# Performance work log

Hardware: AMD Instinct MI355X
Metric: run time of the kernel (lower is better)

## Reference

```python
import jax, jax.numpy as jnp
import numpy as np

# Architecture constants (from RUMamba.__init__ hard-coded Mamba2 config)
D_MODEL = 512
D_STATE = 128
D_CONV = 4
EXPAND = 4
HEADDIM = 32
D_INNER = EXPAND * D_MODEL            # 2048
NHEADS = D_INNER // HEADDIM           # 64
CONV_DIM = D_INNER + 2 * D_STATE      # 2304 (ngroups=1)
D_IN_PROJ = 2 * D_INNER + 2 * D_STATE + NHEADS  # 4416
NUM_CLASS = 2513
BATCH = 4
SEQ = 16


def setup_inputs() -> dict:
    key = jax.random.key(0)
    ks = jax.random.split(key, 8)
    inputs = jax.random.normal(ks[0], (BATCH, SEQ, D_MODEL), jnp.float32)
    in_proj_w = jax.random.normal(ks[1], (D_IN_PROJ, D_MODEL), jnp.float32) * 0.02
    conv_w = jax.random.normal(ks[2], (CONV_DIM, D_CONV), jnp.float32) * 0.2
    conv_b = jnp.zeros((CONV_DIM,), jnp.float32)
    # dt_bias initialized so softplus(dt_bias) ~ U(0.001, 0.1), as in Mamba2
    dt = jax.random.uniform(ks[3], (NHEADS,), jnp.float32, 0.001, 0.1)
    dt_bias = dt + jnp.log(-jnp.expm1(-dt))
    A_log = jnp.log(jax.random.uniform(ks[4], (NHEADS,), jnp.float32, 1.0, 16.0))
    cls_w = jax.random.normal(ks[5], (NUM_CLASS, HEADDIM * D_STATE), jnp.float32) * 0.02
    cls_b = jnp.zeros((NUM_CLASS,), jnp.float32)
    return {"inputs": inputs, "in_proj_w": in_proj_w, "conv_w": conv_w,
            "conv_b": conv_b, "dt_bias": dt_bias, "A_log": A_log,
            "cls_w": cls_w, "cls_b": cls_b}


def reference(inputs, in_proj_w, conv_w, conv_b, dt_bias, A_log, cls_w, cls_b):
    # inputs: (B, S, D) -> (S, B, D) as in forward's permute(1,0,2)
    seq = jnp.transpose(inputs, (1, 0, 2))
    S, B, _ = seq.shape

    # Shared in_proj for both rolling and unrolling (same Mamba math on inputs[t]).
    zxbcdt = jnp.einsum('sbd,ed->sbe', seq, in_proj_w)        # (S,B,4416)
    xBC_raw = zxbcdt[..., D_INNER:D_INNER + CONV_DIM]          # (S,B,2304)
    dt = jax.nn.softplus(zxbcdt[..., -NHEADS:] + dt_bias)      # (S,B,H)
    A = -jnp.exp(A_log)                                        # (H,)
    dA = jnp.exp(dt * A)                                       # (S,B,H)

    # --- Rolling pass: one length-1 Mamba call per timestep, SSM state carried,
    # conv state NOT carried -> causal conv on a length-1 seq uses only last tap.
    xBC_r = jax.nn.silu(xBC_raw * conv_w[:, -1] + conv_b)      # (S,B,2304)
    x_r = xBC_r[..., :D_INNER].reshape(S, B, NHEADS, HEADDIM)  # (S,B,H,P)
    B_r = xBC_r[..., D_INNER:D_INNER + D_STATE]                # (S,B,N)
    dBx = dt[..., None, None] * B_r[:, :, None, None, :] * x_r[..., None]  # (S,B,H,P,N)

    def roll_step(h, inp):
        dA_t, dBx_t = inp
        h = dA_t[..., None, None] * h + dBx_t
        return h, h

    h0 = jnp.zeros((B, NHEADS, HEADDIM, D_STATE), seq.dtype)
    _, states = jax.lax.scan(roll_step, h0, (dA, dBx))         # (S,B,H,P,N)

    # --- Unrolling pass: for each t, feed inputs[t] repeated (S - t + 1) times
    # starting from states[t]. Constant input => conv output only depends on
    # min(step, d_conv-1) via cumulative sums of reversed conv taps.
    cw = jnp.cumsum(conv_w[:, ::-1], axis=1)                   # (2304,4)
    t_idx = jnp.arange(S)

    def unroll_step(h, k):
        w_k = cw[:, jnp.minimum(k, D_CONV - 1)]                # (2304,)
        xBC_k = jax.nn.silu(xBC_raw * w_k + conv_b)            # (S,B,2304)
        x_k = xBC_k[..., :D_INNER].reshape(S, B, NHEADS, HEADDIM)
        B_k = xBC_k[..., D_INNER:D_INNER + D_STATE]
        h_new = dA[..., None, None] * h + \
            dt[..., None, None] * B_k[:, :, None, None, :] * x_k[..., None]
        active = (k <= S - t_idx)[:, None, None, None, None]   # length S - t + 1
        return jnp.where(active, h_new, h), None

    h_fin, _ = jax.lax.scan(unroll_step, states, jnp.arange(S + 1))  # (S,B,H,P,N)

    # Head-reduce to headdim*d_state = 4096 features, classify.
    feats = jnp.mean(h_fin, axis=2).reshape(S, B, HEADDIM * D_STATE)
    feats = jnp.transpose(feats, (1, 0, 2))                    # (B,S,4096)
    y = feats @ cls_w.T + cls_b                                # (B,S,num_class)
    return y
```

## Files before the change

### kernel.cpp

```cpp
#include <hip/hip_runtime.h>
#include <math.h>

#define S_LEN    16
#define NTOK     64
#define DMODEL   512
#define XB_COLS  2176
#define ZX_COLS  2240
#define NCLASS   2513
#define FEATDIM  4096
#define PD_STRIDE 2516
#define APAD     68

typedef float f4v __attribute__((ext_vector_type(4)));

__global__ __launch_bounds__(256) void k_fpart(const float* __restrict__ X,
                                               const float* __restrict__ W,
                                               float* __restrict__ partF) {
    const int tid = threadIdx.x;
    const int kf  = blockIdx.y;
    const int jb  = blockIdx.x * 64;
    const int k0  = kf * 64;

    __shared__ float A[64][64];
    __shared__ float B[64][64];

    {
        const int t  = tid >> 2;
        const int kq = tid & 3;
        const int xrow = (t & 3) * 16 + (t >> 2);
        const int e = (jb + t < XB_COLS) ? (2048 + jb + t) : (2176 + jb + t);
#pragma unroll
        for (int q = 0; q < 4; ++q) {
            const int kk = kq * 16 + q * 4;
            const float4 va = *reinterpret_cast<const float4*>(
                X + (size_t)xrow * DMODEL + k0 + kk);
            A[kk + 0][t] = va.x; A[kk + 1][t] = va.y;
            A[kk + 2][t] = va.z; A[kk + 3][t] = va.w;
            const float4 vb = *reinterpret_cast<const float4*>(
                W + (size_t)e * DMODEL + k0 + kk);
            B[kk + 0][t] = vb.x; B[kk + 1][t] = vb.y;
            B[kk + 2][t] = vb.z; B[kk + 3][t] = vb.w;
        }
    }
    __syncthreads();

    const int ti = tid >> 4;
    const int ci = tid & 15;
    float acc[4][4] = {{0.f}};
#pragma unroll 4
    for (int k = 0; k < 64; ++k) {
        const f4v a = *reinterpret_cast<const f4v*>(&A[k][ti * 4]);
        const f4v b = *reinterpret_cast<const f4v*>(&B[k][ci * 4]);
#pragma unroll
        for (int j = 0; j < 4; ++j)
#pragma unroll
            for (int l = 0; l < 4; ++l)
                acc[j][l] += a[j] * b[l];
    }
#pragma unroll
    for (int jj = 0; jj < 4; ++jj) {
        f4v s; s[0] = acc[jj][0]; s[1] = acc[jj][1];
               s[2] = acc[jj][2]; s[3] = acc[jj][3];
        *reinterpret_cast<f4v*>(
            partF + ((size_t)kf * NTOK + ti * 4 + jj) * ZX_COLS + jb + ci * 4) = s;
    }
}

__global__ __launch_bounds__(256) void k_fepi(const float* __restrict__ partF, int KF,
                                              const float* __restrict__ conv_w,
                                              const float* __restrict__ conv_b,
                                              const float* __restrict__ dt_bias,
                                              const float* __restrict__ A_log,
                                              float* __restrict__ u,
                                              float* __restrict__ aArr,
                                              float* __restrict__ dArr) {
    const int idx = blockIdx.x * 256 + threadIdx.x;
    const int m = idx / ZX_COLS;
    const int j = idx - m * ZX_COLS;
    float acc = 0.f;
    for (int kf = 0; kf < KF; ++kf)
        acc += partF[((size_t)kf * NTOK + m) * ZX_COLS + j];

    if (j < XB_COLS) {
        const float4 cwv = *reinterpret_cast<const float4*>(conv_w + j * 4);
        const float cb = conv_b[j];
        float wk[4];
        wk[0] = cwv.w;
        wk[1] = wk[0] + cwv.z;
        wk[2] = wk[1] + cwv.y;
        wk[3] = wk[2] + cwv.x;
#pragma unroll
        for (int k = 0; k < 4; ++k) {
            const float v = acc * wk[k] + cb;
            u[((size_t)k * NTOK + m) * XB_COLS + j] = v / (1.f + expf(-v));
        }
    } else {
        const int h = j - XB_COLS;
        const float x = acc + dt_bias[h];
        const float d = (x > 20.f) ? x : log1pf(expf(x));
        dArr[m * 64 + h] = d;
        aArr[m * 64 + h] = expf(-d * expf(A_log[h]));
    }
}

__global__ __launch_bounds__(256) void k_feats(const float* __restrict__ u,
                                               const float* __restrict__ aArr,
                                               const float* __restrict__ dArr,
                                               float* __restrict__ feats) {
    const int t = blockIdx.x >> 2;
    const int b = blockIdx.x & 3;
    const int tid = threadIdx.x;
    const int K = 16 - t;
    const int nvec = t + 5;

    __shared__ float q[16][64];
    __shared__ float cu[4][64];
    __shared__ float WV[20][32];
    __shared__ float Bv[20][128];

    if (tid < 64) {
        const int h = tid;
        const int mt = t * 4 + b;
        const float a   = aArr[mt * 64 + h];
        const float dtv = dArr[mt * 64 + h];
        float p = 1.f;
        float c3 = 0.f, c2 = 0.f, c1 = 0.f, c0 = 0.f, cs = 0.f;
        for (int j = 0; j <= K + 1; ++j) {
            if (j <= K - 3) c3 += p;
            if (j == K - 2) c2 = p;
            if (j == K - 1) c1 = p;
            if (j == K)     c0 = p;
            if (j == K + 1) cs = p;
            p *= a;
        }
        cu[0][h] = dtv * c0;
        cu[1][h] = dtv * c1;
        cu[2][h] = dtv * c2;
        cu[3][h] = dtv * c3;
        float prod = 1.f;
        for (int s = t; s >= 0; --s) {
            const int ms = s * 4 + b;
            q[s][h] = cs * prod * dArr[ms * 64 + h];
            prod *= aArr[ms * 64 + h];
        }
    }
    __syncthreads();

    {
        const int i = tid & 31;
        const int vs = tid >> 5;
        for (int v = vs; v < nvec; v += 8) {
            float acc = 0.f;
            if (v <= t) {
                const float* base = u + (size_t)(v * 4 + b) * XB_COLS;
                for (int h = 0; h < 64; ++h) acc += q[v][h] * base[h * 32 + i];
            } else {
                const int kk = v - t - 1;
                const float* base = u + ((size_t)kk * NTOK + t * 4 + b) * XB_COLS;
                for (int h = 0; h < 64; ++h) acc += cu[kk][h] * base[h * 32 + i];
            }
            WV[v][i] = acc;
        }
    }
    for (int x = tid; x < nvec * 128; x += 256) {
        const int v = x >> 7, n = x & 127;
        size_t src;
        if (v <= t) src = (size_t)(v * 4 + b) * XB_COLS + 2048 + n;
        else        src = ((size_t)(v - t - 1) * NTOK + t * 4 + b) * XB_COLS + 2048 + n;
        Bv[v][n] = u[src];
    }
    __syncthreads();

    {
        const int i  = tid >> 3;
        const int n0 = (tid & 7) * 16;
        const int r  = b * 16 + t;
        float acc[16];
#pragma unroll
        for (int nn = 0; nn < 16; ++nn) acc[nn] = 0.f;
        for (int v = 0; v < nvec; ++v) {
            const float wvv = WV[v][i];
#pragma unroll
            for (int nn = 0; nn < 16; ++nn) acc[nn] += wvv * Bv[v][n0 + nn];
        }
        float* dst = feats + (size_t)r * FEATDIM + i * 128 + n0;
#pragma unroll
        for (int qq = 0; qq < 4; ++qq) {
            float4 v4;
            v4.x = acc[qq * 4 + 0] * (1.f / 64.f);
            v4.y = acc[qq * 4 + 1] * (1.f / 64.f);
            v4.z = acc[qq * 4 + 2] * (1.f / 64.f);
            v4.w = acc[qq * 4 + 3] * (1.f / 64.f);
            *reinterpret_cast<float4*>(dst + qq * 4) = v4;
        }
    }
}

__global__ __launch_bounds__(256) void k_cls(const float* __restrict__ feats,
                                             const float* __restrict__ Wc,
                                             float* __restrict__ partialD) {
    const int tid   = threadIdx.x;
    const int lane  = tid & 63;
    const int wv    = tid >> 6;
    const int ks    = blockIdx.y;
    const int cls0  = blockIdx.x * 64;
    const int chunk = FEATDIM / gridDim.y;
    const int nsub  = chunk / 64;

    __shared__ float lds[12288];
    float* A = lds;
    float* B = lds + 64 * APAD;

    const int rq = tid >> 4;
    const int kq = tid & 15;
    int crow[4];
#pragma unroll
    for (int r = 0; r < 4; ++r) {
        int cr = cls0 + rq * 4 + r; if (cr > NCLASS - 1) cr = NCLASS - 1;
        crow[r] = cr;
    }

    const int ti = lane >> 3;
    const int ci = lane & 7;

    float4 pa[4], pb[4];
#define LOADREGS(ST)                                                      \
    do {                                                                  \
        const int k0_ = ks * chunk + (ST) * 64 + kq * 4;                  \
        _Pragma("unroll")                                                 \
        for (int r = 0; r < 4; ++r) {                                     \
            pa[r] = *reinterpret_cast<const float4*>(                     \
                feats + (size_t)(rq * 4 + r) * FEATDIM + k0_);            \
            pb[r] = *reinterpret_cast<const float4*>(                     \
                Wc + (size_t)crow[r] * FEATDIM + k0_);                    \
        }                                                                 \
    } while (0)

    float acc[8][8] = {{0.f}};

    LOADREGS(0);
    for (int st = 0; st < nsub; ++st) {
        __syncthreads();
        {
#pragma unroll
            for (int s = 0; s < 4; ++s) {
                const int kk = kq * 4 + s;
                f4v wa; wa[0] = (&pa[0].x)[s]; wa[1] = (&pa[1].x)[s];
                        wa[2] = (&pa[2].x)[s]; wa[3] = (&pa[3].x)[s];
                *reinterpret_cast<f4v*>(&A[kk * APAD + rq * 4]) = wa;
                f4v wb; wb[0] = (&pb[0].x)[s]; wb[1] = (&pb[1].x)[s];
                        wb[2] = (&pb[2].x)[s]; wb[3] = (&pb[3].x)[s];
                *reinterpret_cast<f4v*>(&B[kk * APAD + rq * 4]) = wb;
            }
        }
        if (st + 1 < nsub) LOADREGS(st + 1);
        __syncthreads();

#pragma unroll
        for (int k = 0; k < 16; ++k) {
            const int kk = wv * 16 + k;
            const f4v a0 = *reinterpret_cast<const f4v*>(&A[kk * APAD + ti * 4]);
            const f4v a1 = *reinterpret_cast<const f4v*>(&A[kk * APAD + 32 + ti * 4]);
            const f4v b0 = *reinterpret_cast<const f4v*>(&B[kk * APAD + ci * 4]);
            const f4v b1 = *reinterpret_cast<const f4v*>(&B[kk * APAD + 32 + ci * 4]);
#pragma unroll
            for (int j = 0; j < 4; ++j) {
#pragma unroll
                for (int l = 0; l < 4; ++l) {
                    acc[j][l]         += a0[j] * b0[l];
                    acc[j][l + 4]     += a0[j] * b1[l];
                    acc[j + 4][l]     += a1[j] * b0[l];
                    acc[j + 4][l + 4] += a1[j] * b1[l];
                }
            }
        }
    }
#undef LOADREGS

    __syncthreads();
    if (wv > 0) {
        const int w = wv - 1;
#pragma unroll
        for (int i = 0; i < 64; ++i)
            lds[w * 4096 + i * 64 + lane] = acc[i >> 3][i & 7];
    }
    __syncthreads();
    if (wv == 0) {
#pragma unroll
        for (int i = 0; i < 64; ++i)
            acc[i >> 3][i & 7] += lds[i * 64 + lane]
                                + lds[4096 + i * 64 + lane]
                                + lds[8192 + i * 64 + lane];

        const size_t obase = (size_t)ks * (NTOK * PD_STRIDE);
#pragma unroll
        for (int ta = 0; ta < 2; ++ta) {
#pragma unroll
            for (int j = 0; j < 4; ++j) {
                const int row = ta * 32 + ti * 4 + j;
#pragma unroll
                for (int cb = 0; cb < 2; ++cb) {
                    const int c = cls0 + cb * 32 + ci * 4;
                    f4v s;
#pragma unroll
                    for (int l = 0; l < 4; ++l) s[l] = acc[ta * 4 + j][cb * 4 + l];
                    float* dst = partialD + obase + (size_t)row * PD_STRIDE + c;
                    if (c + 3 < NCLASS) {
                        *reinterpret_cast<f4v*>(dst) = s;
                    } else {
#pragma unroll
                        for (int l = 0; l < 4; ++l)
                            if (c + l < NCLASS) dst[l] = s[l];
                    }
                }
            }
        }
    }
}

__global__ void k_out(const float* __restrict__ partialD, const float* __restrict__ cls_b,
                      float* __restrict__ out, int NP) {
    const int bx = blockIdx.x;
    const int r  = bx / 10;
    const int c  = (bx % 10) * 256 + threadIdx.x;
    if (c >= NCLASS) return;
    float s = cls_b[c];
    for (int p = 0; p < NP; ++p)
        s += partialD[(size_t)p * (NTOK * PD_STRIDE) + (size_t)r * PD_STRIDE + c];
    out[(size_t)r * NCLASS + c] = s;
}

extern "C" void kernel_launch(void* const* d_in, const int* in_sizes, int n_in,
                              void* d_out, int out_size, void* d_ws, size_t ws_size,
                              hipStream_t stream) {
    const float* inputs  = (const float*)d_in[0];
    const float* in_proj = (const float*)d_in[1];
    const float* conv_w  = (const float*)d_in[2];
    const float* conv_b  = (const float*)d_in[3];
    const float* dt_bias = (const float*)d_in[4];
    const float* A_log   = (const float*)d_in[5];
    const float* cls_w   = (const float*)d_in[6];
    const float* cls_b   = (const float*)d_in[7];
    float* out = (float*)d_out;

    float* ws = (float*)d_ws;
    float* aArr    = ws;
    float* dArr    = ws + 4096;
    float* feats   = ws + 8192;
    float* scr     = ws + 270336;
    float* u       = scr;
    float* partF   = scr + 557056;
    float* partialD = scr;

    int KC;
    if (ws_size >= 11386880u) KC = 16;
    else                      KC = 8;

    k_fpart <<<dim3(35, 8), 256, 0, stream>>>(inputs, in_proj, partF);
    k_fepi  <<<560, 256, 0, stream>>>(partF, 8, conv_w, conv_b, dt_bias, A_log,
                                      u, aArr, dArr);
    k_feats <<<64, 256, 0, stream>>>(u, aArr, dArr, feats);
    k_cls   <<<dim3(40, KC), 256, 0, stream>>>(feats, cls_w, partialD);
    k_out   <<<640, 256, 0, stream>>>(partialD, cls_b, out, KC);
}
```

Baseline: 61.30 us.

## Vectorize epilogue, split feats across more blocks, parallelize cls reduction

The epilogue kernel now processes four columns per thread with vector loads and stores and launches a quarter of the blocks. The feats kernel is split four ways across the headdim dimension, giving 256 blocks instead of 64 so more compute units are used, at the cost of recomputing the per-block q/cu coefficients and reloading B vectors in each block. The classifier's cross-wave reduction is restructured so all four waves write, sum and store half of the tile in two passes, replacing a serial reduction and store done by one wave.

```diff
diff --git a/kernel.cpp b/kernel.cpp
--- a/kernel.cpp
+++ b/kernel.cpp
@@ -74,32 +74,48 @@
                                               float* __restrict__ u,
                                               float* __restrict__ aArr,
                                               float* __restrict__ dArr) {
-    const int idx = blockIdx.x * 256 + threadIdx.x;
-    const int m = idx / ZX_COLS;
-    const int j = idx - m * ZX_COLS;
-    float acc = 0.f;
+    const int idx4 = blockIdx.x * 256 + threadIdx.x;
+    const int m  = idx4 / 560;
+    const int j  = (idx4 - m * 560) * 4;
+
+    f4v acc = {0.f, 0.f, 0.f, 0.f};
     for (int kf = 0; kf < KF; ++kf)
-        acc += partF[((size_t)kf * NTOK + m) * ZX_COLS + j];
+        acc += *reinterpret_cast<const f4v*>(
+            partF + ((size_t)kf * NTOK + m) * ZX_COLS + j);
 
     if (j < XB_COLS) {
-        const float4 cwv = *reinterpret_cast<const float4*>(conv_w + j * 4);
-        const float cb = conv_b[j];
-        float wk[4];
-        wk[0] = cwv.w;
-        wk[1] = wk[0] + cwv.z;
-        wk[2] = wk[1] + cwv.y;
-        wk[3] = wk[2] + cwv.x;
+        float wk[4][4], cb[4];
+#pragma unroll
+        for (int e = 0; e < 4; ++e) {
+            const float4 cwv = *reinterpret_cast<const float4*>(conv_w + (j + e) * 4);
+            cb[e] = conv_b[j + e];
+            wk[e][0] = cwv.w;
+            wk[e][1] = wk[e][0] + cwv.z;
+            wk[e][2] = wk[e][1] + cwv.y;
+            wk[e][3] = wk[e][2] + cwv.x;
+        }
 #pragma unroll
         for (int k = 0; k < 4; ++k) {
-            const float v = acc * wk[k] + cb;
-            u[((size_t)k * NTOK + m) * XB_COLS + j] = v / (1.f + expf(-v));
+            f4v o;
+#pragma unroll
+            for (int e = 0; e < 4; ++e) {
+                const float v = acc[e] * wk[e][k] + cb[e];
+                o[e] = v / (1.f + expf(-v));
+            }
+            *reinterpret_cast<f4v*>(u + ((size_t)k * NTOK + m) * XB_COLS + j) = o;
         }
     } else {
         const int h = j - XB_COLS;
-        const float x = acc + dt_bias[h];
-        const float d = (x > 20.f) ? x : log1pf(expf(x));
-        dArr[m * 64 + h] = d;
-        aArr[m * 64 + h] = expf(-d * expf(A_log[h]));
+        f4v dv, av;
+#pragma unroll
+        for (int e = 0; e < 4; ++e) {
+            const float x = acc[e] + dt_bias[h + e];
+            const float d = (x > 20.f) ? x : log1pf(expf(x));
+            dv[e] = d;
+            av[e] = expf(-d * expf(A_log[h + e]));
+        }
+        *reinterpret_cast<f4v*>(dArr + m * 64 + h) = dv;
+        *reinterpret_cast<f4v*>(aArr + m * 64 + h) = av;
     }
 }
 
@@ -107,15 +123,18 @@
                                                const float* __restrict__ aArr,
                                                const float* __restrict__ dArr,
                                                float* __restrict__ feats) {
-    const int t = blockIdx.x >> 2;
-    const int b = blockIdx.x & 3;
+    const int bx = blockIdx.x;
+    const int g  = bx & 3;
+    const int tb = bx >> 2;
+    const int t  = tb >> 2;
+    const int b  = tb & 3;
     const int tid = threadIdx.x;
     const int K = 16 - t;
     const int nvec = t + 5;
 
     __shared__ float q[16][64];
     __shared__ float cu[4][64];
-    __shared__ float WV[20][32];
+    __shared__ float WV[20][8];
     __shared__ float Bv[20][128];
 
     if (tid < 64) {
@@ -147,9 +166,10 @@
     __syncthreads();
 
     {
-        const int i = tid & 31;
-        const int vs = tid >> 5;
-        for (int v = vs; v < nvec; v += 8) {
+        const int il = tid & 7;
+        const int i  = g * 8 + il;
+        const int vs = tid >> 3;
+        for (int v = vs; v < nvec; v += 32) {
             float acc = 0.f;
             if (v <= t) {
                 const float* base = u + (size_t)(v * 4 + b) * XB_COLS;
@@ -159,7 +179,7 @@
                 const float* base = u + ((size_t)kk * NTOK + t * 4 + b) * XB_COLS;
                 for (int h = 0; h < 64; ++h) acc += cu[kk][h] * base[h * 32 + i];
             }
-            WV[v][i] = acc;
+            WV[v][il] = acc;
         }
     }
     for (int x = tid; x < nvec * 128; x += 256) {
@@ -172,27 +192,20 @@
     __syncthreads();
 
     {
-        const int i  = tid >> 3;
-        const int n0 = (tid & 7) * 16;
+        const int il = tid >> 5;
+        const int i  = g * 8 + il;
+        const int n0 = (tid & 31) * 4;
         const int r  = b * 16 + t;
-        float acc[16];
-#pragma unroll
-        for (int nn = 0; nn < 16; ++nn) acc[nn] = 0.f;
+        float acc[4] = {0.f, 0.f, 0.f, 0.f};
         for (int v = 0; v < nvec; ++v) {
-            const float wvv = WV[v][i];
-#pragma unroll
-            for (int nn = 0; nn < 16; ++nn) acc[nn] += wvv * Bv[v][n0 + nn];
-        }
-        float* dst = feats + (size_t)r * FEATDIM + i * 128 + n0;
-#pragma unroll
-        for (int qq = 0; qq < 4; ++qq) {
-            float4 v4;
-            v4.x = acc[qq * 4 + 0] * (1.f / 64.f);
-            v4.y = acc[qq * 4 + 1] * (1.f / 64.f);
-            v4.z = acc[qq * 4 + 2] * (1.f / 64.f);
-            v4.w = acc[qq * 4 + 3] * (1.f / 64.f);
-            *reinterpret_cast<float4*>(dst + qq * 4) = v4;
-        }
+            const float wvv = WV[v][il];
+#pragma unroll
+            for (int nn = 0; nn < 4; ++nn) acc[nn] += wvv * Bv[v][n0 + nn];
+        }
+        f4v o;
+#pragma unroll
+        for (int nn = 0; nn < 4; ++nn) o[nn] = acc[nn] * (1.f / 64.f);
+        *reinterpret_cast<f4v*>(feats + (size_t)r * FEATDIM + i * 128 + n0) = o;
     }
 }
 
@@ -277,42 +290,37 @@
     }
 #undef LOADREGS
 
-    __syncthreads();
-    if (wv > 0) {
-        const int w = wv - 1;
-#pragma unroll
-        for (int i = 0; i < 64; ++i)
-            lds[w * 4096 + i * 64 + lane] = acc[i >> 3][i & 7];
-    }
-    __syncthreads();
-    if (wv == 0) {
-#pragma unroll
-        for (int i = 0; i < 64; ++i)
-            acc[i >> 3][i & 7] += lds[i * 64 + lane]
-                                + lds[4096 + i * 64 + lane]
-                                + lds[8192 + i * 64 + lane];
-
-        const size_t obase = (size_t)ks * (NTOK * PD_STRIDE);
-#pragma unroll
-        for (int ta = 0; ta < 2; ++ta) {
-#pragma unroll
-            for (int j = 0; j < 4; ++j) {
-                const int row = ta * 32 + ti * 4 + j;
-#pragma unroll
-                for (int cb = 0; cb < 2; ++cb) {
-                    const int c = cls0 + cb * 32 + ci * 4;
-                    f4v s;
-#pragma unroll
-                    for (int l = 0; l < 4; ++l) s[l] = acc[ta * 4 + j][cb * 4 + l];
-                    float* dst = partialD + obase + (size_t)row * PD_STRIDE + c;
-                    if (c + 3 < NCLASS) {
-                        *reinterpret_cast<f4v*>(dst) = s;
-                    } else {
-#pragma unroll
-                        for (int l = 0; l < 4; ++l)
-                            if (c + l < NCLASS) dst[l] = s[l];
-                    }
-                }
+    const size_t obase = (size_t)ks * (NTOK * PD_STRIDE);
+#pragma unroll
+    for (int half = 0; half < 2; ++half) {
+        __syncthreads();
+#pragma unroll
+        for (int i = 0; i < 32; ++i)
+            lds[wv * 2048 + i * 64 + lane] = acc[half * 4 + (i >> 3)][i & 7];
+        __syncthreads();
+
+        float s[8];
+#pragma unroll
+        for (int l = 0; l < 8; ++l)
+            s[l] = lds[          (wv * 8 + l) * 64 + lane]
+                 + lds[2048 +    (wv * 8 + l) * 64 + lane]
+                 + lds[4096 +    (wv * 8 + l) * 64 + lane]
+                 + lds[6144 +    (wv * 8 + l) * 64 + lane];
+
+        const int row = half * 32 + ti * 4 + wv;
+#pragma unroll
+        for (int cb = 0; cb < 2; ++cb) {
+            const int c = cls0 + cb * 32 + ci * 4;
+            f4v v4;
+#pragma unroll
+            for (int l = 0; l < 4; ++l) v4[l] = s[cb * 4 + l];
+            float* dst = partialD + obase + (size_t)row * PD_STRIDE + c;
+            if (c + 3 < NCLASS) {
+                *reinterpret_cast<f4v*>(dst) = v4;
+            } else {
+#pragma unroll
+                for (int l = 0; l < 4; ++l)
+                    if (c + l < NCLASS) dst[l] = v4[l];
             }
         }
     }
@@ -357,9 +365,9 @@
     else                      KC = 8;
 
     k_fpart <<<dim3(35, 8), 256, 0, stream>>>(inputs, in_proj, partF);
-    k_fepi  <<<560, 256, 0, stream>>>(partF, 8, conv_w, conv_b, dt_bias, A_log,
+    k_fepi  <<<140, 256, 0, stream>>>(partF, 8, conv_w, conv_b, dt_bias, A_log,
                                       u, aArr, dArr);
-    k_feats <<<64, 256, 0, stream>>>(u, aArr, dArr, feats);
+    k_feats <<<256, 256, 0, stream>>>(u, aArr, dArr, feats);
     k_cls   <<<dim3(40, KC), 256, 0, stream>>>(feats, cls_w, partialD);
     k_out   <<<640, 256, 0, stream>>>(partialD, cls_b, out, KC);
 }
```

Result: no change. 60.23 us (-1.8%).
